# Kernel tuning notes

Hardware: AMD Instinct MI355X
Metric: run time of the kernel (lower is better)

Reference implementation:

```python
import jax, jax.numpy as jnp
import numpy as np

NUM_NODES = 1_200_000
NUM_FILLER = 200_000
NUM_PHYS = NUM_NODES - NUM_FILLER  # 1,000,000 physical nodes
NUM_MOVABLE = 900_000
NBX = NBY = 512
XL, XH, YL, YH = 0.0, 1000.0, 0.0, 1000.0
BSX = (XH - XL) / NBX
BSY = (YH - YL) / NBY
PIN_STRETCH = 1.4142135623730951
UNIT_PIN_CAP = 0.05
MAX_RATE = 1.5
MIN_RATE = 1.0 / MAX_RATE
K = 5  # max bins overlapped per dimension (span<=4.0, bin~1.95)


def _overlap_terms(lo, hi, bin_size, origin, nb):
    # lo, hi: [n] interval per node. Returns bin indices [n,K] and overlap lengths [n,K].
    il = jnp.clip(jnp.floor((lo - origin) / bin_size).astype(jnp.int32), 0, nb - 1)
    idx = il[:, None] + jnp.arange(K, dtype=jnp.int32)[None, :]
    valid = idx < nb
    idx = jnp.clip(idx, 0, nb - 1)
    b_lo = origin + idx.astype(lo.dtype) * bin_size
    ov = jnp.maximum(jnp.minimum(hi[:, None], b_lo + bin_size) - jnp.maximum(lo[:, None], b_lo), 0.0)
    return idx, jnp.where(valid, ov, 0.0)


def _forward(pos, node_size_x, node_size_y, flat_node2pin_start_map):
    P = NUM_PHYS
    sx, sy = node_size_x[:P], node_size_y[:P]
    # stretched half sizes: at least half a stretched bin
    hx = 0.5 * jnp.maximum(BSX * PIN_STRETCH, sx)
    hy = 0.5 * jnp.maximum(BSY * PIN_STRETCH, sy)
    cx = pos[:P] + 0.5 * sx
    cy = pos[NUM_NODES:NUM_NODES + P] + 0.5 * sy
    pw = (flat_node2pin_start_map[1:P + 1] - flat_node2pin_start_map[:P]).astype(pos.dtype)
    density = pw / (4.0 * hx * hy)  # pins per unit area over stretched bbox

    # stage 1: scatter stretched-bbox pin density into bin map
    ix, ovx = _overlap_terms(cx - hx, cx + hx, BSX, XL, NBX)  # [P,K]
    iy, ovy = _overlap_terms(cy - hy, cy + hy, BSY, YL, NBY)  # [P,K]
    contrib = ovx[:, :, None] * ovy[:, None, :] * density[:, None, None]  # [P,K,K]
    flat_idx = (ix[:, :, None] * NBY + iy[:, None, :]).reshape(-1)
    pin_map = jnp.zeros(NBX * NBY, dtype=pos.dtype).at[flat_idx].add(contrib.reshape(-1))

    # stage 2: pin utilization per bin, clamped adjust rate
    util = jnp.clip(pin_map / (BSX * BSY * UNIT_PIN_CAP), MIN_RATE, MAX_RATE)

    # stage 3: per movable node, integrate utilization over its (unstretched) bbox
    M = NUM_MOVABLE
    x_lo = pos[:M]
    x_hi = x_lo + node_size_x[:M]
    y_lo = pos[NUM_NODES:NUM_NODES + M]
    y_hi = y_lo + node_size_y[:M]
    jx, wx = _overlap_terms(x_lo, x_hi, BSX, XL, NBX)  # [M,K]
    jy, wy = _overlap_terms(y_lo, y_hi, BSY, YL, NBY)  # [M,K]
    u = util[jx[:, :, None] * NBY + jy[:, None, :]]  # [M,K,K]
    instance_pin_area = jnp.sum(wx[:, :, None] * wy[:, None, :] * u, axis=(1, 2))
    return instance_pin_area


def setup_inputs() -> dict:
    key = jax.random.key(0)
    k1, k2, k3, k4 = jax.random.split(key, 4)
    node_size_x = jax.random.uniform(k1, (NUM_NODES,), jnp.float32, 1.0, 4.0)
    node_size_y = jnp.full((NUM_NODES,), 2.0, jnp.float32)  # row height
    px = jax.random.uniform(k2, (NUM_NODES,), jnp.float32, 0.0, 995.0)
    py = jax.random.uniform(k3, (NUM_NODES,), jnp.float32, 0.0, 995.0)
    pos = jnp.concatenate([px, py])
    pin_counts = jax.random.randint(k4, (NUM_PHYS,), 1, 9, jnp.int32)
    flat = jnp.concatenate([jnp.zeros(1, jnp.int32), jnp.cumsum(pin_counts).astype(jnp.int32)])
    return {"pos": pos, "node_size_x": node_size_x, "node_size_y": node_size_y,
            "flat_node2pin_start_map": flat}


def reference(pos, node_size_x, node_size_y, flat_node2pin_start_map):
    return _forward(pos, node_size_x, node_size_y, flat_node2pin_start_map)
```

## Files before the change

kernel.cpp:

```cpp
#include <hip/hip_runtime.h>

#define NUM_NODES   1200000
#define NUM_FILLER  200000
#define NUM_PHYS    (NUM_NODES - NUM_FILLER)
#define NUM_MOVABLE 900000
#define NBX 512
#define NBY 512
#define NBINS (NBX * NBY)
#define BSX 1.953125f
#define BSY 1.953125f
#define PIN_STRETCH 1.4142135623730951f
#define CAP 0.19073486328125f
#define INV_CAP (1.0f / 0.19073486328125f)
#define MAX_RATE 1.5f
#define MIN_RATE (1.0f/1.5f)
#define K 5

#define TBITS   5
#define TSZ     32
#define TDIM    16
#define NTILES  (TDIM * TDIM)
#define HALO    (K - 1)
#define LTS     (TSZ + HALO)
#define NXCD    8
#define SBLK    1024
#define NPB     4096
#define IPT     (NPB / SBLK)
#define NBLK    ((NUM_PHYS + NPB - 1) / NPB)
#define CAPX    1024

__device__ __forceinline__ int bin_lo(float lo) {
    int il = (int)floorf(lo / BSX);
    return min(max(il, 0), NBX - 1);
}

__global__ __launch_bounds__(SBLK) void sort_phys(
    const float* __restrict__ pos,
    const float* __restrict__ nsx,
    const float* __restrict__ nsy,
    const int*   __restrict__ flat,
    int*         __restrict__ cur,
    float4*      __restrict__ rec,
    float*       __restrict__ pin)
{
    __shared__ int cnt[NTILES];
    __shared__ int basep[NTILES];
    int tid = threadIdx.x;
    if (tid < NTILES) cnt[tid] = 0;
    for (int i = blockIdx.x * SBLK + tid; i < NBINS; i += NBLK * SBLK)
        pin[i] = 0.0f;
    __syncthreads();

    unsigned xcc;
    asm volatile("s_getreg_b32 %0, hwreg(HW_REG_XCC_ID, 0, 32)" : "=s"(xcc));
    xcc &= (NXCD - 1);

    float cxv[IPT], cyv[IPT], hxv[IPT], hyv[IPT];
    int pwv[IPT], tl[IPT];
    int base = blockIdx.x * NPB;
    #pragma unroll
    for (int it = 0; it < IPT; ++it) {
        int i = base + it * SBLK + tid;
        tl[it] = -1;
        if (i < NUM_PHYS) {
            float sxv = nsx[i], syv = nsy[i];
            float hx = 0.5f * fmaxf(BSX * PIN_STRETCH, sxv);
            float hy = 0.5f * fmaxf(BSY * PIN_STRETCH, syv);
            float cx = pos[i] + 0.5f * sxv;
            float cy = pos[NUM_NODES + i] + 0.5f * syv;
            cxv[it] = cx; cyv[it] = cy; hxv[it] = hx; hyv[it] = hy;
            pwv[it] = flat[i + 1] - flat[i];
            int t = ((bin_lo(cx - hx) >> TBITS) << 4) | (bin_lo(cy - hy) >> TBITS);
            tl[it] = t;
            atomicAdd(&cnt[t], 1);
        }
    }
    __syncthreads();
    if (tid < NTILES) {
        int c = cnt[tid];
        basep[tid] = (c > 0) ? atomicAdd(&cur[tid * NXCD + xcc], c) : 0;
    }
    __syncthreads();
    #pragma unroll
    for (int it = 0; it < IPT; ++it) {
        int t = tl[it];
        if (t >= 0) {
            int s = atomicAdd(&basep[t], 1);
            if (s < CAPX) {
                unsigned pwm1 = (unsigned)(pwv[it] - 1) & 7u;
                unsigned ux = __float_as_uint(cxv[it]) | ((pwm1 & 1u) << 31);
                unsigned uy = __float_as_uint(cyv[it]) | (((pwm1 >> 1) & 1u) << 31);
                unsigned uz = __float_as_uint(hxv[it]) | (((pwm1 >> 2) & 1u) << 31);
                rec[((size_t)t * NXCD + xcc) * CAPX + s] =
                    make_float4(__uint_as_float(ux), __uint_as_float(uy),
                                __uint_as_float(uz), hyv[it]);
            }
        }
    }
}

__global__ __launch_bounds__(1024) void accumulate_tiles(
    const float4* __restrict__ rec,
    const int*    __restrict__ cur,
    float*        __restrict__ pin)
{
    __shared__ float tileA[LTS * LTS];
    __shared__ int pref[NXCD + 1];
    int tid = threadIdx.x;
    int t = blockIdx.x;
    int bx0 = (t >> 4) * TSZ, by0 = (t & 15) * TSZ;

    for (int i = tid; i < LTS * LTS; i += 1024) tileA[i] = 0.0f;
    if (tid == 0) {
        int s = 0; pref[0] = 0;
        for (int x = 0; x < NXCD; ++x) {
            s += min(cur[t * NXCD + x], CAPX);
            pref[x + 1] = s;
        }
    }
    __syncthreads();

    int total = pref[NXCD];
    size_t tb = (size_t)t * NXCD * CAPX;
    for (int k = tid; k < total; k += 1024) {
        int x = 0;
        while (k >= pref[x + 1]) ++x;
        float4 r = rec[tb + (size_t)x * CAPX + (k - pref[x])];
        unsigned ux = __float_as_uint(r.x), uy = __float_as_uint(r.y),
                 uz = __float_as_uint(r.z);
        float pw = (float)(1 + (int)((ux >> 31) | ((uy >> 31) << 1) | ((uz >> 31) << 2)));
        float cx = __uint_as_float(ux & 0x7fffffffu);
        float cy = __uint_as_float(uy & 0x7fffffffu);
        float hx = __uint_as_float(uz & 0x7fffffffu);
        float hy = r.w;
        float d = pw / (4.0f * hx * hy);
        float lox = cx - hx, hix = cx + hx;
        float loy = cy - hy, hiy = cy + hy;
        int il = bin_lo(lox), jl = bin_lo(loy);
        int ie = min(min((int)floorf(hix / BSX), NBX - 1), il + HALO);
        int je = min(min((int)floorf(hiy / BSY), NBY - 1), jl + HALO);
        int lr = il - bx0, lc = jl - by0;
        for (int a = il; a <= ie; ++a) {
            float blo = (float)a * BSX;
            float ox = fmaxf(fminf(hix, blo + BSX) - fmaxf(lox, blo), 0.0f);
            int rowb = (lr + (a - il)) * LTS + lc;
            for (int b2 = jl; b2 <= je; ++b2) {
                float blo2 = (float)b2 * BSY;
                float oy = fmaxf(fminf(hiy, blo2 + BSY) - fmaxf(loy, blo2), 0.0f);
                float cc = ox * oy * d;
                if (cc != 0.0f) atomicAdd(&tileA[rowb + (b2 - jl)], cc);
            }
        }
    }
    __syncthreads();
    for (int i = tid; i < LTS * LTS; i += 1024) {
        float v = tileA[i];
        int r = i / LTS, c = i % LTS;
        int gx = bx0 + r, gy = by0 + c;
        if (gx >= NBX || gy >= NBY) continue;
        bool interior = (r >= HALO) && (r < TSZ) && (c >= HALO) && (c < TSZ);
        if (interior) {
            if (v != 0.0f) pin[gx * NBY + gy] = v;
        } else {
            if (v != 0.0f) atomicAdd(&pin[gx * NBY + gy], v);
        }
    }
}

__global__ __launch_bounds__(256) void gather_pin_area(
    const float* __restrict__ pos,
    const float* __restrict__ nsx,
    const float* __restrict__ nsy,
    const float* __restrict__ pin,
    float*       __restrict__ out)
{
    int m = blockIdx.x * blockDim.x + threadIdx.x;
    if (m >= NUM_MOVABLE) return;

    float xlo = pos[m];
    float xhi = xlo + nsx[m];
    float ylo = pos[NUM_NODES + m];
    float yhi = ylo + nsy[m];

    int xb = min(bin_lo(xlo), NBX - 4);
    int yb = min(bin_lo(ylo), NBY - 3);

    float u[4][3];
    #pragma unroll
    for (int a = 0; a < 4; ++a) {
        const float* __restrict__ row = pin + (xb + a) * NBY + yb;
        u[a][0] = row[0]; u[a][1] = row[1]; u[a][2] = row[2];
    }

    float wx[4], wy[3];
    #pragma unroll
    for (int kx = 0; kx < 4; ++kx) {
        float blo = (float)(xb + kx) * BSX;
        wx[kx] = fmaxf(fminf(xhi, blo + BSX) - fmaxf(xlo, blo), 0.0f);
    }
    #pragma unroll
    for (int ky = 0; ky < 3; ++ky) {
        float blo = (float)(yb + ky) * BSY;
        wy[ky] = fmaxf(fminf(yhi, blo + BSY) - fmaxf(ylo, blo), 0.0f);
    }

    float acc = 0.0f;
    #pragma unroll
    for (int a = 0; a < 4; ++a)
        #pragma unroll
        for (int b = 0; b < 3; ++b) {
            float uc = fminf(fmaxf(u[a][b] * INV_CAP, MIN_RATE), MAX_RATE);
            acc += wx[a] * wy[b] * uc;
        }
    out[m] = acc;
}

__global__ __launch_bounds__(256) void scatter_pin_map_agent(
    const float* __restrict__ pos,
    const float* __restrict__ nsx,
    const float* __restrict__ nsy,
    const int*   __restrict__ flat,
    float*       __restrict__ map)
{
    int p = blockIdx.x * blockDim.x + threadIdx.x;
    if (p >= NUM_PHYS) return;
    float sx = nsx[p], sy = nsy[p];
    float hx = 0.5f * fmaxf(BSX * PIN_STRETCH, sx);
    float hy = 0.5f * fmaxf(BSY * PIN_STRETCH, sy);
    float cx = pos[p] + 0.5f * sx;
    float cy = pos[NUM_NODES + p] + 0.5f * sy;
    float pw = (float)(flat[p + 1] - flat[p]);
    float density = pw / (4.0f * hx * hy);
    float lox = cx - hx, hixv = cx + hx;
    float loy = cy - hy, hiyv = cy + hy;
    int il = bin_lo(lox), jl = bin_lo(loy);
    int ie = min(min((int)floorf(hixv / BSX), NBX - 1), il + K - 1);
    int je = min(min((int)floorf(hiyv / BSY), NBY - 1), jl + K - 1);
    for (int a = il; a <= ie; ++a) {
        float blo = (float)a * BSX;
        float ox = fmaxf(fminf(hixv, blo + BSX) - fmaxf(lox, blo), 0.0f);
        for (int b = jl; b <= je; ++b) {
            float blo2 = (float)b * BSY;
            float oy = fmaxf(fminf(hiyv, blo2 + BSY) - fmaxf(loy, blo2), 0.0f);
            float c = ox * oy * density;
            if (c != 0.0f) atomicAdd(&map[a * NBY + b], c);
        }
    }
}

__global__ __launch_bounds__(256) void gather_general(
    const float* __restrict__ pos,
    const float* __restrict__ nsx,
    const float* __restrict__ nsy,
    const float* __restrict__ pin,
    float*       __restrict__ out)
{
    int m = blockIdx.x * blockDim.x + threadIdx.x;
    if (m >= NUM_MOVABLE) return;
    float xlo = pos[m];
    float xhi = xlo + nsx[m];
    float ylo = pos[NUM_NODES + m];
    float yhi = ylo + nsy[m];
    int il = bin_lo(xlo);
    int ie = min(min((int)floorf(xhi / BSX), NBX - 1), il + K - 1);
    int jl = bin_lo(ylo);
    int je = min(min((int)floorf(yhi / BSY), NBY - 1), jl + K - 1);
    float acc = 0.0f;
    for (int a = il; a <= ie; ++a) {
        float blo = (float)a * BSX;
        float wxv = fmaxf(fminf(xhi, blo + BSX) - fmaxf(xlo, blo), 0.0f);
        const float* __restrict__ row = pin + a * NBY;
        for (int b2 = jl; b2 <= je; ++b2) {
            float blo2 = (float)b2 * BSY;
            float wyv = fmaxf(fminf(yhi, blo2 + BSY) - fmaxf(ylo, blo2), 0.0f);
            float uc = fminf(fmaxf(row[b2] * INV_CAP, MIN_RATE), MAX_RATE);
            acc += wxv * wyv * uc;
        }
    }
    out[m] = acc;
}

extern "C" void kernel_launch(void* const* d_in, const int* in_sizes, int n_in,
                              void* d_out, int out_size, void* d_ws, size_t ws_size,
                              hipStream_t stream) {
    const float* pos  = (const float*)d_in[0];
    const float* nsx  = (const float*)d_in[1];
    const float* nsy  = (const float*)d_in[2];
    const int*   flat = (const int*)d_in[3];
    float* out = (float*)d_out;

    const size_t NSLOT = (size_t)NTILES * NXCD * CAPX;
    char* wsb = (char*)d_ws;
    float*  pin = (float*)wsb;
    int*    cur = (int*)(wsb + (size_t)NBINS * 4);
    float4* rec = (float4*)(wsb + (size_t)NBINS * 4 + 32768);
    size_t needed = (size_t)NBINS * 4 + 32768 + NSLOT * 16;

    dim3 blk(256);
    if (ws_size >= needed) {
        hipMemsetAsync(cur, 0, (size_t)NTILES * NXCD * sizeof(int), stream);
        sort_phys<<<NBLK, dim3(SBLK), 0, stream>>>(pos, nsx, nsy, flat, cur, rec, pin);
        accumulate_tiles<<<NTILES, dim3(1024), 0, stream>>>(rec, cur, pin);
        gather_pin_area<<<(NUM_MOVABLE + 255) / 256, blk, 0, stream>>>(pos, nsx, nsy, pin, out);
    } else {
        hipMemsetAsync(pin, 0, (size_t)NBINS * 4, stream);
        scatter_pin_map_agent<<<(NUM_PHYS + 255) / 256, blk, 0, stream>>>(pos, nsx, nsy, flat, pin);
        gather_general<<<(NUM_MOVABLE + 255) / 256, blk, 0, stream>>>(pos, nsx, nsy, pin, out);
    }
}
```

Measured before the change: 140.3 us.

## Stage tile-sorted records in LDS and vectorize sort and gather loads

The binning kernel now reads four nodes per thread with float4 loads. It orders the block's records by tile in shared memory using a prefix scan, then writes them out so each tile's records are contiguous. This replaces scattered per-record global writes with more coalesced ones. The gather kernel also processes four movable nodes per thread with float4 input loads and a float4 output store. The costs are a 64KB LDS staging buffer, extra syncthreads in the scan, and lower occupancy for the sort kernel.

```diff
diff --git a/kernel.cpp b/kernel.cpp
--- a/kernel.cpp
+++ b/kernel.cpp
@@ -25,13 +25,21 @@
 #define NXCD    8
 #define SBLK    1024
 #define NPB     4096
-#define IPT     (NPB / SBLK)
 #define NBLK    ((NUM_PHYS + NPB - 1) / NPB)
 #define CAPX    1024
 
 __device__ __forceinline__ int bin_lo(float lo) {
     int il = (int)floorf(lo / BSX);
     return min(max(il, 0), NBX - 1);
+}
+
+__device__ __forceinline__ float4 pack_rec(float cx, float cy, float hx, float hy, int pw) {
+    unsigned pwm1 = (unsigned)(pw - 1) & 7u;
+    unsigned ux = __float_as_uint(cx) | ((pwm1 & 1u) << 31);
+    unsigned uy = __float_as_uint(cy) | (((pwm1 >> 1) & 1u) << 31);
+    unsigned uz = __float_as_uint(hx) | (((pwm1 >> 2) & 1u) << 31);
+    return make_float4(__uint_as_float(ux), __uint_as_float(uy),
+                       __uint_as_float(uz), hy);
 }
 
 __global__ __launch_bounds__(SBLK) void sort_phys(
@@ -43,11 +51,18 @@
     float4*      __restrict__ rec,
     float*       __restrict__ pin)
 {
-    __shared__ int cnt[NTILES];
-    __shared__ int basep[NTILES];
+    __shared__ int    cnt[NTILES];
+    __shared__ int    pref[NTILES];
+    __shared__ int    exc[NTILES];
+    __shared__ int    lofs[NTILES];
+    __shared__ int    gbase[NTILES];
+    __shared__ float4 stage[NPB];
+    __shared__ unsigned char tileOf[NPB];
+
     int tid = threadIdx.x;
+    int bid = blockIdx.x;
     if (tid < NTILES) cnt[tid] = 0;
-    for (int i = blockIdx.x * SBLK + tid; i < NBINS; i += NBLK * SBLK)
+    for (int i = bid * SBLK + tid; i < NBINS; i += NBLK * SBLK)
         pin[i] = 0.0f;
     __syncthreads();
 
@@ -55,47 +70,76 @@
     asm volatile("s_getreg_b32 %0, hwreg(HW_REG_XCC_ID, 0, 32)" : "=s"(xcc));
     xcc &= (NXCD - 1);
 
-    float cxv[IPT], cyv[IPT], hxv[IPT], hyv[IPT];
-    int pwv[IPT], tl[IPT];
-    int base = blockIdx.x * NPB;
-    #pragma unroll
-    for (int it = 0; it < IPT; ++it) {
-        int i = base + it * SBLK + tid;
-        tl[it] = -1;
-        if (i < NUM_PHYS) {
-            float sxv = nsx[i], syv = nsy[i];
-            float hx = 0.5f * fmaxf(BSX * PIN_STRETCH, sxv);
-            float hy = 0.5f * fmaxf(BSY * PIN_STRETCH, syv);
-            float cx = pos[i] + 0.5f * sxv;
-            float cy = pos[NUM_NODES + i] + 0.5f * syv;
-            cxv[it] = cx; cyv[it] = cy; hxv[it] = hx; hyv[it] = hy;
-            pwv[it] = flat[i + 1] - flat[i];
+    int q = bid * SBLK + tid;
+    bool valid = (4 * q + 3) < NUM_PHYS;
+    float4 r4[4];
+    int tl[4] = {-1, -1, -1, -1};
+    if (valid) {
+        const float4* pos4  = (const float4*)pos;
+        const float4* posy4 = (const float4*)(pos + NUM_NODES);
+        const float4* nsx4  = (const float4*)nsx;
+        const float4* nsy4  = (const float4*)nsy;
+        float4 px = pos4[q], py = posy4[q];
+        float4 sx = nsx4[q], sy = nsy4[q];
+        int4 f4 = ((const int4*)flat)[q];
+        int f5 = flat[4 * q + 4];
+        int pw0 = f4.y - f4.x, pw1 = f4.z - f4.y, pw2 = f4.w - f4.z, pw3 = f5 - f4.w;
+        float pxs[4] = {px.x, px.y, px.z, px.w};
+        float pys[4] = {py.x, py.y, py.z, py.w};
+        float sxs[4] = {sx.x, sx.y, sx.z, sx.w};
+        float sys[4] = {sy.x, sy.y, sy.z, sy.w};
+        int   pws[4] = {pw0, pw1, pw2, pw3};
+        #pragma unroll
+        for (int j = 0; j < 4; ++j) {
+            float hx = 0.5f * fmaxf(BSX * PIN_STRETCH, sxs[j]);
+            float hy = 0.5f * fmaxf(BSY * PIN_STRETCH, sys[j]);
+            float cx = pxs[j] + 0.5f * sxs[j];
+            float cy = pys[j] + 0.5f * sys[j];
+            r4[j] = pack_rec(cx, cy, hx, hy, pws[j]);
             int t = ((bin_lo(cx - hx) >> TBITS) << 4) | (bin_lo(cy - hy) >> TBITS);
-            tl[it] = t;
+            tl[j] = t;
             atomicAdd(&cnt[t], 1);
         }
     }
     __syncthreads();
+
     if (tid < NTILES) {
         int c = cnt[tid];
-        basep[tid] = (c > 0) ? atomicAdd(&cur[tid * NXCD + xcc], c) : 0;
+        gbase[tid] = (c > 0) ? atomicAdd(&cur[tid * NXCD + xcc], c) : 0;
+        pref[tid] = c;
     }
     __syncthreads();
     #pragma unroll
-    for (int it = 0; it < IPT; ++it) {
-        int t = tl[it];
-        if (t >= 0) {
-            int s = atomicAdd(&basep[t], 1);
-            if (s < CAPX) {
-                unsigned pwm1 = (unsigned)(pwv[it] - 1) & 7u;
-                unsigned ux = __float_as_uint(cxv[it]) | ((pwm1 & 1u) << 31);
-                unsigned uy = __float_as_uint(cyv[it]) | (((pwm1 >> 1) & 1u) << 31);
-                unsigned uz = __float_as_uint(hxv[it]) | (((pwm1 >> 2) & 1u) << 31);
-                rec[((size_t)t * NXCD + xcc) * CAPX + s] =
-                    make_float4(__uint_as_float(ux), __uint_as_float(uy),
-                                __uint_as_float(uz), hyv[it]);
-            }
-        }
+    for (int off = 1; off < NTILES; off <<= 1) {
+        int v = (tid < NTILES && tid >= off) ? pref[tid - off] : 0;
+        __syncthreads();
+        if (tid < NTILES) pref[tid] += v;
+        __syncthreads();
+    }
+    if (tid < NTILES) {
+        int e = pref[tid] - cnt[tid];
+        exc[tid] = e;
+        lofs[tid] = e;
+    }
+    __syncthreads();
+
+    if (valid) {
+        #pragma unroll
+        for (int j = 0; j < 4; ++j) {
+            int t = tl[j];
+            int r = atomicAdd(&lofs[t], 1);
+            stage[r] = r4[j];
+            tileOf[r] = (unsigned char)t;
+        }
+    }
+    __syncthreads();
+
+    int total = pref[NTILES - 1];
+    for (int k = tid; k < total; k += SBLK) {
+        int t = tileOf[k];
+        int dst = gbase[t] + (k - exc[t]);
+        if (dst < CAPX)
+            rec[((size_t)t * NXCD + xcc) * CAPX + dst] = stage[k];
     }
 }
 
@@ -174,45 +218,55 @@
     const float* __restrict__ pin,
     float*       __restrict__ out)
 {
-    int m = blockIdx.x * blockDim.x + threadIdx.x;
-    if (m >= NUM_MOVABLE) return;
-
-    float xlo = pos[m];
-    float xhi = xlo + nsx[m];
-    float ylo = pos[NUM_NODES + m];
-    float yhi = ylo + nsy[m];
-
-    int xb = min(bin_lo(xlo), NBX - 4);
-    int yb = min(bin_lo(ylo), NBY - 3);
-
-    float u[4][3];
+    int q = blockIdx.x * blockDim.x + threadIdx.x;
+    if (q >= NUM_MOVABLE / 4) return;
+
+    float4 xl4 = ((const float4*)pos)[q];
+    float4 yl4 = ((const float4*)(pos + NUM_NODES))[q];
+    float4 sx4 = ((const float4*)nsx)[q];
+    float4 sy4 = ((const float4*)nsy)[q];
+
+    float xls[4] = {xl4.x, xl4.y, xl4.z, xl4.w};
+    float yls[4] = {yl4.x, yl4.y, yl4.z, yl4.w};
+    float sxs[4] = {sx4.x, sx4.y, sx4.z, sx4.w};
+    float sys[4] = {sy4.x, sy4.y, sy4.z, sy4.w};
+    float res[4];
+
     #pragma unroll
-    for (int a = 0; a < 4; ++a) {
-        const float* __restrict__ row = pin + (xb + a) * NBY + yb;
-        u[a][0] = row[0]; u[a][1] = row[1]; u[a][2] = row[2];
-    }
-
-    float wx[4], wy[3];
-    #pragma unroll
-    for (int kx = 0; kx < 4; ++kx) {
-        float blo = (float)(xb + kx) * BSX;
-        wx[kx] = fmaxf(fminf(xhi, blo + BSX) - fmaxf(xlo, blo), 0.0f);
-    }
-    #pragma unroll
-    for (int ky = 0; ky < 3; ++ky) {
-        float blo = (float)(yb + ky) * BSY;
-        wy[ky] = fmaxf(fminf(yhi, blo + BSY) - fmaxf(ylo, blo), 0.0f);
-    }
-
-    float acc = 0.0f;
-    #pragma unroll
-    for (int a = 0; a < 4; ++a)
-        #pragma unroll
-        for (int b = 0; b < 3; ++b) {
-            float uc = fminf(fmaxf(u[a][b] * INV_CAP, MIN_RATE), MAX_RATE);
-            acc += wx[a] * wy[b] * uc;
-        }
-    out[m] = acc;
+    for (int j = 0; j < 4; ++j) {
+        float xlo = xls[j], xhi = xlo + sxs[j];
+        float ylo = yls[j], yhi = ylo + sys[j];
+        int xb = min(bin_lo(xlo), NBX - 4);
+        int yb = min(bin_lo(ylo), NBY - 3);
+
+        float u[4][3];
+        #pragma unroll
+        for (int a = 0; a < 4; ++a) {
+            const float* __restrict__ row = pin + (xb + a) * NBY + yb;
+            u[a][0] = row[0]; u[a][1] = row[1]; u[a][2] = row[2];
+        }
+        float wx[4], wy[3];
+        #pragma unroll
+        for (int kx = 0; kx < 4; ++kx) {
+            float blo = (float)(xb + kx) * BSX;
+            wx[kx] = fmaxf(fminf(xhi, blo + BSX) - fmaxf(xlo, blo), 0.0f);
+        }
+        #pragma unroll
+        for (int ky = 0; ky < 3; ++ky) {
+            float blo = (float)(yb + ky) * BSY;
+            wy[ky] = fmaxf(fminf(yhi, blo + BSY) - fmaxf(ylo, blo), 0.0f);
+        }
+        float acc = 0.0f;
+        #pragma unroll
+        for (int a = 0; a < 4; ++a)
+            #pragma unroll
+            for (int b = 0; b < 3; ++b) {
+                float uc = fminf(fmaxf(u[a][b] * INV_CAP, MIN_RATE), MAX_RATE);
+                acc += wx[a] * wy[b] * uc;
+            }
+        res[j] = acc;
+    }
+    ((float4*)out)[q] = make_float4(res[0], res[1], res[2], res[3]);
 }
 
 __global__ __launch_bounds__(256) void scatter_pin_map_agent(
@@ -301,7 +355,7 @@
         hipMemsetAsync(cur, 0, (size_t)NTILES * NXCD * sizeof(int), stream);
         sort_phys<<<NBLK, dim3(SBLK), 0, stream>>>(pos, nsx, nsy, flat, cur, rec, pin);
         accumulate_tiles<<<NTILES, dim3(1024), 0, stream>>>(rec, cur, pin);
-        gather_pin_area<<<(NUM_MOVABLE + 255) / 256, blk, 0, stream>>>(pos, nsx, nsy, pin, out);
+        gather_pin_area<<<(NUM_MOVABLE / 4 + 255) / 256, blk, 0, stream>>>(pos, nsx, nsy, pin, out);
     } else {
         hipMemsetAsync(pin, 0, (size_t)NBINS * 4, stream);
         scatter_pin_map_agent<<<(NUM_PHYS + 255) / 256, blk, 0, stream>>>(pos, nsx, nsy, flat, pin);
```

Measured after the change: 140.2 us. About the same (-0.0%).
